# Optimization experiments

Hardware: AMD Instinct MI355X
Metric: run time of the kernel (lower is better)

Reference implementation:

```python
import jax, jax.numpy as jnp
import numpy as np

NEG_INF = -1e9  # matches masked_fill value -1000000000.0
SLOPE = 0.2     # LeakyReLU negative slope


def setup_inputs() -> dict:
    key = jax.random.key(0)
    k1, k2, k3, k4 = jax.random.split(key, 4)
    B, N, Fin, Fout = 16, 1024, 256, 256
    h = jax.random.normal(k1, (B, N, Fin), dtype=jnp.float32)
    adj = jax.random.randint(k2, (B, N, N), 0, 2, dtype=jnp.int32)
    W = jax.random.normal(k3, (Fin, Fout), dtype=jnp.float32) * (1.0 / np.sqrt(Fin))
    a = jax.random.normal(k4, (2 * Fout,), dtype=jnp.float32) * (1.0 / np.sqrt(2 * Fout))
    return {"h": h, "adj": adj, "W": W, "a": a}


def reference(h, adj, W, a):
    # h: [B,N,Fin], adj: [B,N,N] (0/1), W: [Fin,Fout], a: [2*Fout]
    Fout = W.shape[1]
    Wh = jnp.einsum("bnf,fo->bno", h, W)            # [B,N,Fout]
    a1, a2 = a[:Fout], a[Fout:]
    # e[b,i,j] = leakyrelu( Wh[b,i]·a1 + Wh[b,j]·a2 )  == a(cat(Wh_i, Wh_j))
    f1 = Wh @ a1                                     # [B,N]
    f2 = Wh @ a2                                     # [B,N]
    e = jax.nn.leaky_relu(f1[:, :, None] + f2[:, None, :], negative_slope=SLOPE)
    e = jnp.where(adj == 0, NEG_INF, e)              # mask non-edges
    attention = jax.nn.softmax(e, axis=-1)           # [B,N,N]
    # dropout is identity at eval / p=0
    h_prime = jnp.einsum("bij,bjo->bio", attention, Wh)  # [B,N,Fout]
    return h_prime
```

## Files before the change

### kernel.cpp

```cpp
#include <hip/hip_runtime.h>

typedef __attribute__((ext_vector_type(8))) short bf16x8;
typedef __attribute__((ext_vector_type(4))) float f32x4;
typedef __attribute__((ext_vector_type(4))) float fvec4;

__device__ __forceinline__ unsigned short f2bf(float x) {
    unsigned int u = __float_as_uint(x);
    u += 0x7FFFu + ((u >> 16) & 1u);
    return (unsigned short)(u >> 16);
}

__device__ __forceinline__ void gl_lds16(const void* g, void* l) {
    __builtin_amdgcn_global_load_lds(
        (__attribute__((address_space(1))) void*)((void*)g),
        (__attribute__((address_space(3))) void*)l, 16, 0, 0);
}

#define SFENCE __builtin_amdgcn_sched_barrier(0)

__global__ __launch_bounds__(256) void prep(const float* __restrict__ W,
                                            short* __restrict__ WbT) {
    __shared__ float tile[32][33];
    const int t = threadIdx.x;
    const int bx = blockIdx.x & 7, by = blockIdx.x >> 3;
    const int r0 = by * 32, c0 = bx * 32;
    const int lr = t >> 5, lc = t & 31;
#pragma unroll
    for (int q = 0; q < 4; ++q)
        tile[q * 8 + lr][lc] = W[(r0 + q * 8 + lr) * 256 + c0 + lc];
    __syncthreads();
#pragma unroll
    for (int q = 0; q < 4; ++q)
        WbT[(c0 + q * 8 + lr) * 256 + r0 + lc] = (short)f2bf(tile[lc][q * 8 + lr]);
}

__global__ __launch_bounds__(256, 4) void setup2(const float* __restrict__ h,
                                                 const short* __restrict__ WbT,
                                                 const float* __restrict__ a,
                                                 const int* __restrict__ adj,
                                                 short* __restrict__ WhT,
                                                 float* __restrict__ f1,
                                                 float* __restrict__ f2,
                                                 unsigned long long* __restrict__ bits) {
    __shared__ short hA[32][264];
    __shared__ float sp[2][4][32];
    const int t = threadIdx.x;
    const int wid = t >> 6, lane = t & 63;

    if (blockIdx.x >= 512) {
        const int row = (blockIdx.x - 512) * 4 + wid;
        const int* arow = adj + (size_t)row * 1024;
        unsigned long long myword = 0ull;
#pragma unroll
        for (int w = 0; w < 16; ++w) {
            int v = __builtin_nontemporal_load(arow + w * 64 + lane);
            unsigned long long bal = __ballot(v != 0);
            if (lane == w) myword = bal;
        }
        if (lane < 16) bits[(size_t)row * 16 + lane] = myword;
        return;
    }

    const int quad = lane >> 4, l15 = lane & 15;
    const int m0 = blockIdx.x * 32;

#pragma unroll
    for (int rr = 0; rr < 2; ++rr) {
        const int r = rr * 16 + (t >> 4), c0 = (t & 15) * 16;
        const float* hp = h + (size_t)(m0 + r) * 256 + c0;
        fvec4 v0 = __builtin_nontemporal_load((const fvec4*)(hp + 0));
        fvec4 v1 = __builtin_nontemporal_load((const fvec4*)(hp + 4));
        fvec4 v2 = __builtin_nontemporal_load((const fvec4*)(hp + 8));
        fvec4 v3 = __builtin_nontemporal_load((const fvec4*)(hp + 12));
        bf16x8 w0, w1;
#pragma unroll
        for (int u = 0; u < 4; ++u) {
            w0[u]     = (short)f2bf(v0[u]);
            w0[u + 4] = (short)f2bf(v1[u]);
            w1[u]     = (short)f2bf(v2[u]);
            w1[u + 4] = (short)f2bf(v3[u]);
        }
        *(bf16x8*)&hA[r][c0] = w0;
        *(bf16x8*)&hA[r][c0 + 8] = w1;
    }
    __syncthreads();

    f32x4 acc[2][4] = {};
#pragma unroll
    for (int kt = 0; kt < 8; ++kt) {
        const int k0 = kt * 32;
        bf16x8 bv[4];
#pragma unroll
        for (int ft = 0; ft < 4; ++ft)
            bv[ft] = *(const bf16x8*)(WbT + (size_t)(wid * 64 + ft * 16 + l15) * 256 + k0 + quad * 8);
        bf16x8 a0 = *(const bf16x8*)&hA[l15][k0 + quad * 8];
        bf16x8 a1 = *(const bf16x8*)&hA[16 + l15][k0 + quad * 8];
#pragma unroll
        for (int ft = 0; ft < 4; ++ft) {
            acc[0][ft] = __builtin_amdgcn_mfma_f32_16x16x32_bf16(a0, bv[ft], acc[0][ft], 0, 0, 0);
            acc[1][ft] = __builtin_amdgcn_mfma_f32_16x16x32_bf16(a1, bv[ft], acc[1][ft], 0, 0, 0);
        }
    }

    const int b = m0 >> 10;
#pragma unroll
    for (int mf = 0; mf < 2; ++mf) {
        const int il0 = (m0 & 1023) + mf * 16 + quad * 4;
        const int T = il0 >> 6, jw = il0 & 63;
#pragma unroll
        for (int ft = 0; ft < 4; ++ft) {
            const int f = wid * 64 + ft * 16 + l15;
            ushort4 pk;
            pk.x = f2bf(acc[mf][ft][0]);
            pk.y = f2bf(acc[mf][ft][1]);
            pk.z = f2bf(acc[mf][ft][2]);
            pk.w = f2bf(acc[mf][ft][3]);
            *(ushort4*)(WhT + ((size_t)b << 18) + T * 16384 + (size_t)f * 64 + jw) = pk;
        }
    }

    float a1v[4], a2v[4];
#pragma unroll
    for (int ft = 0; ft < 4; ++ft) {
        a1v[ft] = a[wid * 64 + ft * 16 + l15];
        a2v[ft] = a[256 + wid * 64 + ft * 16 + l15];
    }
    float p1[2][4] = {}, p2[2][4] = {};
#pragma unroll
    for (int mf = 0; mf < 2; ++mf)
#pragma unroll
        for (int ft = 0; ft < 4; ++ft)
#pragma unroll
            for (int r = 0; r < 4; ++r) {
                p1[mf][r] += acc[mf][ft][r] * a1v[ft];
                p2[mf][r] += acc[mf][ft][r] * a2v[ft];
            }
#pragma unroll
    for (int off = 1; off < 16; off <<= 1)
#pragma unroll
        for (int mf = 0; mf < 2; ++mf)
#pragma unroll
            for (int r = 0; r < 4; ++r) {
                p1[mf][r] += __shfl_xor(p1[mf][r], off);
                p2[mf][r] += __shfl_xor(p2[mf][r], off);
            }
    if (l15 == 0)
#pragma unroll
        for (int mf = 0; mf < 2; ++mf)
#pragma unroll
            for (int r = 0; r < 4; ++r) {
                sp[0][wid][mf * 16 + quad * 4 + r] = p1[mf][r];
                sp[1][wid][mf * 16 + quad * 4 + r] = p2[mf][r];
            }
    __syncthreads();
    if (t < 32) {
        f1[m0 + t] = sp[0][0][t] + sp[0][1][t] + sp[0][2][t] + sp[0][3][t];
        f2[m0 + t] = sp[1][0][t] + sp[1][1][t] + sp[1][2][t] + sp[1][3][t];
    }
}

__global__ __launch_bounds__(512, 2) void fused_agg(const unsigned long long* __restrict__ bitsG,
                                                    const float* __restrict__ f1g,
                                                    const float* __restrict__ f2g,
                                                    const short* __restrict__ WhT,
                                                    float* __restrict__ out) {
    __shared__ short Bs[3][256 * 64];
    __shared__ short Ps[2][64 * 64];
    __shared__ unsigned long long bitsS[16 * 64];
    __shared__ float f2s[1024];
    __shared__ float lred[512];
    __shared__ float linv[64];

    const int t = threadIdx.x;
    const int wid = t >> 6, lane = t & 63;
    const int quad = lane >> 4, l15 = lane & 15;

    const int id = blockIdx.x;
    const int xcd = id & 7, rest = id >> 3;
    const int b = xcd + 8 * (rest & 1);
    const int m0 = (rest >> 1) * 64;

    const short* Wb = WhT + ((size_t)b << 18);

    {
        const unsigned long long* bsrc = bitsG + (size_t)((b << 10) + m0) * 16;
        ulonglong2 bv = ((const ulonglong2*)bsrc)[t];
        const int g0 = 2 * t, g1 = 2 * t + 1;
        bitsS[(g0 & 15) * 64 + (g0 >> 4)] = bv.x;
        bitsS[(g1 & 15) * 64 + (g1 >> 4)] = bv.y;
        ((float2*)f2s)[t] = ((const float2*)(f2g + (b << 10)))[t];
    }
    const int pr = t >> 3, ps = t & 7;
    const float f1r = f1g[(b << 10) + m0 + pr];
    __syncthreads();

    auto stage = [&](int T, short* buf) {
        const short* src = Wb + T * 16384;
#pragma unroll
        for (int q = 0; q < 4; ++q) {
            const int c = t + 512 * q;
            const int rr = c >> 3;
            const int sl = (c & 7) ^ (rr & 7);
            gl_lds16(src + rr * 64 + sl * 8, buf + c * 8);
        }
    };

    float lacc = 0.f;
    auto pgen = [&](int T, short* pbuf) {
        unsigned int m8 = (unsigned int)(bitsS[T * 64 + pr] >> (ps * 8)) & 0xffu;
        float4 fa = *(const float4*)(f2s + T * 64 + ps * 8);
        float4 fb = *(const float4*)(f2s + T * 64 + ps * 8 + 4);
        float xv[8] = {fa.x, fa.y, fa.z, fa.w, fb.x, fb.y, fb.z, fb.w};
        bf16x8 pw;
#pragma unroll
        for (int u = 0; u < 8; ++u) {
            float x = f1r + xv[u];
            x = fmaxf(x, 0.2f * x);
            float pv = ((m8 >> u) & 1u) ? __expf(x) : 0.f;
            lacc += pv;
            pw[u] = (short)f2bf(pv);
        }
        *(bf16x8*)(pbuf + pr * 64 + ((ps ^ (pr & 7)) * 8)) = pw;
    };

    const int wm = wid >> 2, wn = wid & 3;
    const int mh = wm * 32, nq = wn * 64;
    f32x4 acc[2][4] = {};

    auto step = [&](const short* pbuf, const short* bbuf) {
#pragma unroll
        for (int kt = 0; kt < 2; ++kt) {
            const int w = kt * 4 + quad;
            bf16x8 av[2], bv[4];
#pragma unroll
            for (int mf = 0; mf < 2; ++mf) {
                const int ra = mh + mf * 16 + l15;
                av[mf] = *(const bf16x8*)(pbuf + ra * 64 + ((w ^ (ra & 7)) * 8));
            }
#pragma unroll
            for (int nf = 0; nf < 4; ++nf) {
                const int rb = nq + nf * 16 + l15;
                bv[nf] = *(const bf16x8*)(bbuf + rb * 64 + ((w ^ (rb & 7)) * 8));
            }
#pragma unroll
            for (int mf = 0; mf < 2; ++mf)
#pragma unroll
                for (int nf = 0; nf < 4; ++nf)
                    acc[mf][nf] = __builtin_amdgcn_mfma_f32_16x16x32_bf16(av[mf], bv[nf], acc[mf][nf], 0, 0, 0);
        }
    };

    stage(0, Bs[0]);
    stage(1, Bs[1]);
    pgen(0, Ps[0]);
    asm volatile("s_waitcnt lgkmcnt(0)" ::: "memory");
    SFENCE;
    asm volatile("s_waitcnt vmcnt(4)" ::: "memory");
    SFENCE;
    __builtin_amdgcn_s_barrier();
    SFENCE;

#pragma unroll
    for (int T = 0; T < 16; ++T) {
        if (T < 14) stage(T + 2, Bs[(T + 2) % 3]);
        if (T < 15) pgen(T + 1, Ps[(T + 1) & 1]);
        __builtin_amdgcn_s_setprio(1);
        step(Ps[T & 1], Bs[T % 3]);
        __builtin_amdgcn_s_setprio(0);
        asm volatile("s_waitcnt lgkmcnt(0)" ::: "memory");
        SFENCE;
        if (T < 14) {
            asm volatile("s_waitcnt vmcnt(4)" ::: "memory");
        } else if (T == 14) {
            asm volatile("s_waitcnt vmcnt(0)" ::: "memory");
        }
        SFENCE;
        __builtin_amdgcn_s_barrier();
        SFENCE;
    }

    lred[t] = lacc;
    __syncthreads();
    if (t < 64) {
        const float* lp = lred + t * 8;
        linv[t] = 1.0f / (((lp[0] + lp[1]) + (lp[2] + lp[3])) +
                          ((lp[4] + lp[5]) + (lp[6] + lp[7])));
    }
    __syncthreads();

#pragma unroll
    for (int mf = 0; mf < 2; ++mf) {
        const int il = mh + mf * 16 + quad * 4;
        const float i0 = linv[il], i1 = linv[il + 1];
        const float i2 = linv[il + 2], i3 = linv[il + 3];
#pragma unroll
        for (int nf = 0; nf < 4; ++nf) {
            float* op = out + (size_t)((b << 10) + m0 + il) * 256 + nq + nf * 16 + l15;
            op[0]   = acc[mf][nf][0] * i0;
            op[256] = acc[mf][nf][1] * i1;
            op[512] = acc[mf][nf][2] * i2;
            op[768] = acc[mf][nf][3] * i3;
        }
    }
}

extern "C" void kernel_launch(void* const* d_in, const int* in_sizes, int n_in,
                              void* d_out, int out_size, void* d_ws, size_t ws_size,
                              hipStream_t stream) {
    const float* h   = (const float*)d_in[0];
    const int*   adj = (const int*)d_in[1];
    const float* W   = (const float*)d_in[2];
    const float* a   = (const float*)d_in[3];
    float* out = (float*)d_out;

    short* WbT = (short*)d_ws;
    float* f1  = (float*)(WbT + 65536);
    float* f2  = f1 + 16384;
    short* WhT = (short*)(f2 + 16384);
    unsigned long long* bits =
        (unsigned long long*)(WhT + 16 * 256 * 1024);

    prep<<<64, 256, 0, stream>>>(W, WbT);
    setup2<<<4608, 256, 0, stream>>>(h, WbT, a, adj, WhT, f1, f2, bits);
    fused_agg<<<256, 512, 0, stream>>>(bits, f1, f2, WhT, out);
}
```

Baseline: 142.8 us.

## Make aggregation waves independent with per-wave staging and register-resident P

Each wave now stages its own 64-column slice of Wh into a private double buffer and builds its attention probabilities directly in MFMA A-operand registers. This removes the shared P buffer and all block-wide barriers in the main loop. Row sums are reduced with lane shuffles instead of through shared memory. In exchange, each wave recomputes the exp values for its 32 rows, so the exp work is repeated four times across the column-split waves. The change to launch bounds and LDS footprint may also change occupancy.

Result: slower. 154.8 us (+8.4%).

```diff
diff --git a/kernel.cpp b/kernel.cpp
--- a/kernel.cpp
+++ b/kernel.cpp
@@ -159,21 +159,20 @@
     }
 }
 
-__global__ __launch_bounds__(512, 2) void fused_agg(const unsigned long long* __restrict__ bitsG,
-                                                    const float* __restrict__ f1g,
-                                                    const float* __restrict__ f2g,
-                                                    const short* __restrict__ WhT,
-                                                    float* __restrict__ out) {
-    __shared__ short Bs[3][256 * 64];
-    __shared__ short Ps[2][64 * 64];
+__global__ __launch_bounds__(512) void fused_agg(const unsigned long long* __restrict__ bitsG,
+                                                 const float* __restrict__ f1g,
+                                                 const float* __restrict__ f2g,
+                                                 const short* __restrict__ WhT,
+                                                 float* __restrict__ out) {
+    __shared__ short Bs[8][2][4096];
     __shared__ unsigned long long bitsS[16 * 64];
     __shared__ float f2s[1024];
-    __shared__ float lred[512];
-    __shared__ float linv[64];
 
     const int t = threadIdx.x;
     const int wid = t >> 6, lane = t & 63;
     const int quad = lane >> 4, l15 = lane & 15;
+    const int wm = wid >> 2, wn = wid & 3;
+    const int mh = wm * 32, nq = wn * 64;
 
     const int id = blockIdx.x;
     const int xcd = id & 7, rest = id >> 3;
@@ -184,122 +183,118 @@
 
     {
         const unsigned long long* bsrc = bitsG + (size_t)((b << 10) + m0) * 16;
-        ulonglong2 bv = ((const ulonglong2*)bsrc)[t];
+        ulonglong2 bv2 = ((const ulonglong2*)bsrc)[t];
         const int g0 = 2 * t, g1 = 2 * t + 1;
-        bitsS[(g0 & 15) * 64 + (g0 >> 4)] = bv.x;
-        bitsS[(g1 & 15) * 64 + (g1 >> 4)] = bv.y;
+        bitsS[(g0 & 15) * 64 + (g0 >> 4)] = bv2.x;
+        bitsS[(g1 & 15) * 64 + (g1 >> 4)] = bv2.y;
         ((float2*)f2s)[t] = ((const float2*)(f2g + (b << 10)))[t];
     }
-    const int pr = t >> 3, ps = t & 7;
-    const float f1r = f1g[(b << 10) + m0 + pr];
+    const float f1a = f1g[(b << 10) + m0 + mh + l15];
+    const float f1b = f1g[(b << 10) + m0 + mh + 16 + l15];
     __syncthreads();
 
-    auto stage = [&](int T, short* buf) {
-        const short* src = Wb + T * 16384;
-#pragma unroll
-        for (int q = 0; q < 4; ++q) {
-            const int c = t + 512 * q;
-            const int rr = c >> 3;
-            const int sl = (c & 7) ^ (rr & 7);
-            gl_lds16(src + rr * 64 + sl * 8, buf + c * 8);
+    short* bufA = &Bs[wid][0][0];
+    short* bufB = &Bs[wid][1][0];
+
+    auto stageTo = [&](int T, short* dst) {
+        const short* src = Wb + (size_t)T * 16384 + (size_t)nq * 64;
+#pragma unroll
+        for (int j = 0; j < 8; ++j) {
+            const int c = j * 64 + lane;
+            const int rr = c >> 3, sl = (c & 7) ^ (rr & 7);
+            gl_lds16(src + rr * 64 + sl * 8, dst + c * 8);
         }
     };
 
-    float lacc = 0.f;
-    auto pgen = [&](int T, short* pbuf) {
-        unsigned int m8 = (unsigned int)(bitsS[T * 64 + pr] >> (ps * 8)) & 0xffu;
-        float4 fa = *(const float4*)(f2s + T * 64 + ps * 8);
-        float4 fb = *(const float4*)(f2s + T * 64 + ps * 8 + 4);
-        float xv[8] = {fa.x, fa.y, fa.z, fa.w, fb.x, fb.y, fb.z, fb.w};
-        bf16x8 pw;
-#pragma unroll
-        for (int u = 0; u < 8; ++u) {
-            float x = f1r + xv[u];
-            x = fmaxf(x, 0.2f * x);
-            float pv = ((m8 >> u) & 1u) ? __expf(x) : 0.f;
-            lacc += pv;
-            pw[u] = (short)f2bf(pv);
-        }
-        *(bf16x8*)(pbuf + pr * 64 + ((ps ^ (pr & 7)) * 8)) = pw;
-    };
-
-    const int wm = wid >> 2, wn = wid & 3;
-    const int mh = wm * 32, nq = wn * 64;
     f32x4 acc[2][4] = {};
-
-    auto step = [&](const short* pbuf, const short* bbuf) {
-#pragma unroll
-        for (int kt = 0; kt < 2; ++kt) {
-            const int w = kt * 4 + quad;
-            bf16x8 av[2], bv[4];
-#pragma unroll
-            for (int mf = 0; mf < 2; ++mf) {
-                const int ra = mh + mf * 16 + l15;
-                av[mf] = *(const bf16x8*)(pbuf + ra * 64 + ((w ^ (ra & 7)) * 8));
-            }
+    float ls0 = 0.f, ls1 = 0.f;
+
+    stageTo(0, bufA);
+    stageTo(1, bufB);
+
+    auto body = [&](int T, short* bufRead, bool doStage) {
+        bf16x8 bv[2][4];
+#pragma unroll
+        for (int kt = 0; kt < 2; ++kt)
 #pragma unroll
             for (int nf = 0; nf < 4; ++nf) {
-                const int rb = nq + nf * 16 + l15;
-                bv[nf] = *(const bf16x8*)(bbuf + rb * 64 + ((w ^ (rb & 7)) * 8));
-            }
-#pragma unroll
-            for (int mf = 0; mf < 2; ++mf)
-#pragma unroll
-                for (int nf = 0; nf < 4; ++nf)
-                    acc[mf][nf] = __builtin_amdgcn_mfma_f32_16x16x32_bf16(av[mf], bv[nf], acc[mf][nf], 0, 0, 0);
-        }
-    };
-
-    stage(0, Bs[0]);
-    stage(1, Bs[1]);
-    pgen(0, Ps[0]);
-    asm volatile("s_waitcnt lgkmcnt(0)" ::: "memory");
-    SFENCE;
-    asm volatile("s_waitcnt vmcnt(4)" ::: "memory");
-    SFENCE;
-    __builtin_amdgcn_s_barrier();
-    SFENCE;
-
-#pragma unroll
-    for (int T = 0; T < 16; ++T) {
-        if (T < 14) stage(T + 2, Bs[(T + 2) % 3]);
-        if (T < 15) pgen(T + 1, Ps[(T + 1) & 1]);
-        __builtin_amdgcn_s_setprio(1);
-        step(Ps[T & 1], Bs[T % 3]);
-        __builtin_amdgcn_s_setprio(0);
+                const int rb = nf * 16 + l15;
+                const int w = kt * 4 + quad;
+                bv[kt][nf] = *(const bf16x8*)(bufRead + rb * 64 + ((w ^ (rb & 7)) * 8));
+            }
         asm volatile("s_waitcnt lgkmcnt(0)" ::: "memory");
         SFENCE;
-        if (T < 14) {
-            asm volatile("s_waitcnt vmcnt(4)" ::: "memory");
-        } else if (T == 14) {
-            asm volatile("s_waitcnt vmcnt(0)" ::: "memory");
-        }
+        if (doStage) stageTo(T + 2, bufRead);
+
+        const unsigned long long w0 = bitsS[T * 64 + mh + l15];
+        const unsigned long long w1 = bitsS[T * 64 + mh + 16 + l15];
+        bf16x8 pa[2][2];
+#pragma unroll
+        for (int kt = 0; kt < 2; ++kt) {
+            const float* fp = f2s + T * 64 + kt * 32 + quad * 8;
+            float4 fa = *(const float4*)fp;
+            float4 fb = *(const float4*)(fp + 4);
+            float xv[8] = {fa.x, fa.y, fa.z, fa.w, fb.x, fb.y, fb.z, fb.w};
+            const int sh = kt * 32 + quad * 8;
+            const unsigned int m80 = (unsigned int)(w0 >> sh) & 0xffu;
+            const unsigned int m81 = (unsigned int)(w1 >> sh) & 0xffu;
+#pragma unroll
+            for (int u = 0; u < 8; ++u) {
+                float x0 = f1a + xv[u];
+                x0 = fmaxf(x0, 0.2f * x0);
+                float p0 = ((m80 >> u) & 1u) ? __expf(x0) : 0.f;
+                ls0 += p0;
+                pa[0][kt][u] = (short)f2bf(p0);
+                float x1 = f1b + xv[u];
+                x1 = fmaxf(x1, 0.2f * x1);
+                float p1 = ((m81 >> u) & 1u) ? __expf(x1) : 0.f;
+                ls1 += p1;
+                pa[1][kt][u] = (short)f2bf(p1);
+            }
+        }
+
+        __builtin_amdgcn_s_setprio(1);
+#pragma unroll
+        for (int kt = 0; kt < 2; ++kt)
+#pragma unroll
+            for (int mf = 0; mf < 2; ++mf)
+#pragma unroll
+                for (int nf = 0; nf < 4; ++nf)
+                    acc[mf][nf] = __builtin_amdgcn_mfma_f32_16x16x32_bf16(
+                        mf ? pa[1][kt] : pa[0][kt], bv[kt][nf], acc[mf][nf], 0, 0, 0);
+        __builtin_amdgcn_s_setprio(0);
+    };
+
+    for (int Tp = 0; Tp < 7; ++Tp) {
+        const int T0 = Tp * 2;
+        asm volatile("s_waitcnt vmcnt(8)" ::: "memory");
         SFENCE;
-        __builtin_amdgcn_s_barrier();
+        body(T0, bufA, true);
+        asm volatile("s_waitcnt vmcnt(8)" ::: "memory");
         SFENCE;
-    }
-
-    lred[t] = lacc;
-    __syncthreads();
-    if (t < 64) {
-        const float* lp = lred + t * 8;
-        linv[t] = 1.0f / (((lp[0] + lp[1]) + (lp[2] + lp[3])) +
-                          ((lp[4] + lp[5]) + (lp[6] + lp[7])));
-    }
-    __syncthreads();
+        body(T0 + 1, bufB, true);
+    }
+    asm volatile("s_waitcnt vmcnt(8)" ::: "memory");
+    SFENCE;
+    body(14, bufA, false);
+    asm volatile("s_waitcnt vmcnt(0)" ::: "memory");
+    SFENCE;
+    body(15, bufB, false);
+
+    ls0 += __shfl_xor(ls0, 16); ls0 += __shfl_xor(ls0, 32);
+    ls1 += __shfl_xor(ls1, 16); ls1 += __shfl_xor(ls1, 32);
 
 #pragma unroll
     for (int mf = 0; mf < 2; ++mf) {
         const int il = mh + mf * 16 + quad * 4;
-        const float i0 = linv[il], i1 = linv[il + 1];
-        const float i2 = linv[il + 2], i3 = linv[il + 3];
-#pragma unroll
-        for (int nf = 0; nf < 4; ++nf) {
-            float* op = out + (size_t)((b << 10) + m0 + il) * 256 + nq + nf * 16 + l15;
-            op[0]   = acc[mf][nf][0] * i0;
-            op[256] = acc[mf][nf][1] * i1;
-            op[512] = acc[mf][nf][2] * i2;
-            op[768] = acc[mf][nf][3] * i3;
+#pragma unroll
+        for (int r = 0; r < 4; ++r) {
+            const float s = __shfl(mf ? ls1 : ls0, quad * 4 + r);
+            const float inv = 1.0f / s;
+            float* op = out + (size_t)((b << 10) + m0 + il + r) * 256 + nq + l15;
+#pragma unroll
+            for (int nf = 0; nf < 4; ++nf)
+                op[nf * 16] = acc[mf][nf][r] * inv;
         }
     }
 }
```
